# Optimization experiments

Measured on AMD Instinct MI355X. Metric: run time of the kernel, lower is better.

## Reference

```python
import jax, jax.numpy as jnp
import numpy as np

N_NODES = 50000
N_EDGES = 800000
IN_FEAT = 256
HEADS = 8
D_K = 64


def setup_inputs() -> dict:
    key = jax.random.key(0)
    ks = jax.random.split(key, 6)
    x = jax.random.normal(ks[0], (N_NODES, IN_FEAT), dtype=jnp.float32)
    edge_index = jax.random.randint(ks[1], (2, N_EDGES), 0, N_NODES, dtype=jnp.int32)
    # xavier-uniform linear weights, stored as [in, out] for x @ W
    limit = float(np.sqrt(6.0 / (IN_FEAT + HEADS * D_K)))
    Wq = jax.random.uniform(ks[2], (IN_FEAT, HEADS * D_K), jnp.float32, -limit, limit)
    Wk = jax.random.uniform(ks[3], (IN_FEAT, HEADS * D_K), jnp.float32, -limit, limit)
    Wv = jax.random.uniform(ks[4], (IN_FEAT, HEADS * D_K), jnp.float32, -limit, limit)
    D = jax.random.uniform(ks[5], (HEADS, D_K), jnp.float32, -1.0, 1.0)
    return {"x": x, "edge_index": edge_index, "Wq": Wq, "Wk": Wk, "Wv": Wv, "D": D}


def reference(x, edge_index, Wq, Wk, Wv, D):
    N = x.shape[0]
    H, dk = D.shape
    scale = 1.0 / np.sqrt(dk)

    Q = (x @ Wq).reshape(N, H, dk)
    K = (x @ Wk).reshape(N, H, dk)
    V = (x @ Wv).reshape(N, H, dk)

    row, col = edge_index[0], edge_index[1]
    Ke = K[row]          # [E, H, dk]
    Qe = Q[col]          # [E, H, dk] (for self edges col==row so Q[col]==Q[row])
    diff = Ke - Qe
    s_edge = jnp.einsum('ehd,hd->eh', diff * diff, D)   # diagonal Mahalanobis
    s_self = jnp.einsum('ehd,hd->eh', Ke * Qe, D)       # self-loop score
    scores = jnp.where((row == col)[:, None], s_self, s_edge)
    scores = jax.nn.leaky_relu(scores * scale, negative_slope=0.2)

    # segment softmax over destination node `row` (PyG softmax semantics)
    smax = jax.ops.segment_max(scores, row, num_segments=N)
    smax = jnp.where(jnp.isfinite(smax), smax, 0.0)     # nodes with no incoming edges
    ex = jnp.exp(scores - smax[row])
    denom = jax.ops.segment_sum(ex, row, num_segments=N)
    alpha = ex / (denom[row] + 1e-16)                   # [E, H]

    out = jax.ops.segment_sum(alpha[:, :, None] * V[col], row, num_segments=N)
    return out.reshape(N, H * dk)
```

## Files before the change

### kernel.cpp

```cpp
#include <hip/hip_runtime.h>
#include <hip/hip_bf16.h>

#define N_NODES 50000
#define N_PAD   50176
#define N_EDGES 800000
#define IN_FEAT 256
#define HEADS 8
#define D_K 64
#define HD 512

typedef __hip_bfloat16 bf16;
typedef unsigned int u32;

using bf16x8 = __attribute__((ext_vector_type(8))) short;
using f32x4  = __attribute__((ext_vector_type(4))) float;

#define WS_Q       0
#define WS_K       51200000
#define WS_V       102400000
#define WS_OFFSETS 153600000
#define WS_CURSOR  153800192
#define WS_DEG     154000192
#define WS_CSR     154200192
#define WS_SQ2     157400192
#define WS_AUX     159000192

#define DOUT_XB 0
#define DOUT_WT 25690112

#define SCAN_BLOCKS 49
#define EA_BLOCKS   1024

#define VMCNT0()   asm volatile("s_waitcnt vmcnt(0)" ::: "memory")
#define LGKMCNT0() asm volatile("s_waitcnt lgkmcnt(0)" ::: "memory")

__device__ __forceinline__ float bflo(u32 u) { return __uint_as_float(u << 16); }
__device__ __forceinline__ float bfhi(u32 u) { return __uint_as_float(u & 0xffff0000u); }

__device__ __forceinline__ void gload16(const void* g, void* l)
{
    __builtin_amdgcn_global_load_lds(
        (const __attribute__((address_space(1))) unsigned int*)g,
        (__attribute__((address_space(3))) unsigned int*)l,
        16, 0, 0);
}

__global__ __launch_bounds__(256) void convert_x(
    const float* __restrict__ x, bf16* __restrict__ xb)
{
    const int t   = blockIdx.x * 256 + threadIdx.x;
    const int row = t >> 5;
    const int c8  = (t & 31) * 8;
    if (row >= N_PAD) return;
    alignas(16) bf16 tmp[8];
    if (row < N_NODES) {
        const float* p = x + (size_t)row * IN_FEAT + c8;
        float4 a = *(const float4*)p;
        float4 b = *(const float4*)(p + 4);
        tmp[0] = __float2bfloat16(a.x); tmp[1] = __float2bfloat16(a.y);
        tmp[2] = __float2bfloat16(a.z); tmp[3] = __float2bfloat16(a.w);
        tmp[4] = __float2bfloat16(b.x); tmp[5] = __float2bfloat16(b.y);
        tmp[6] = __float2bfloat16(b.z); tmp[7] = __float2bfloat16(b.w);
    } else {
#pragma unroll
        for (int i = 0; i < 8; ++i) tmp[i] = __float2bfloat16(0.f);
    }
    *(uint4*)(xb + (size_t)row * IN_FEAT + c8) = *(const uint4*)tmp;
}

__global__ __launch_bounds__(256) void convert_w(
    const float* __restrict__ Wq, const float* __restrict__ Wk, const float* __restrict__ Wv,
    bf16* __restrict__ Wt)
{
    const int t = blockIdx.x * 256 + threadIdx.x;
    if (t >= 3 * 512 * 256) return;
    const int mat = t >> 17;
    const int r   = t & 131071;
    const int n   = r >> 8;
    const int k   = r & 255;
    const float* W = (mat == 0) ? Wq : (mat == 1) ? Wk : Wv;
    Wt[t] = __float2bfloat16(W[k * HD + n]);
}

__global__ __launch_bounds__(256) void mfma_qkv(
    const bf16* __restrict__ xb, const bf16* __restrict__ Wt,
    bf16* __restrict__ Qb, bf16* __restrict__ Kb, bf16* __restrict__ Vb)
{
    __shared__ uint4 Ab4[512];
    __shared__ uint4 Bb4[512];
    char* AbB = (char*)Ab4;
    char* BbB = (char*)Bb4;

    const int tid  = threadIdx.x;
    const int lane = tid & 63;
    const int wid  = tid >> 6;
    const int wr   = wid >> 1;
    const int wc   = wid & 1;

    const int m0  = blockIdx.x * 128;
    const int n0  = blockIdx.y * 128;
    const int mat = blockIdx.z;
    const bf16* __restrict__ wt = Wt + (size_t)mat * 512 * 256;
    bf16* __restrict__ outp = (mat == 0) ? Qb : (mat == 1) ? Kb : Vb;

    const int rch  = lane >> 2;
    const int slot = (lane & 3) ^ (rch & 3);
    const int sc0  = wid;
    const int sc1  = wid + 4;
    const size_t arow0 = (size_t)(m0 + sc0 * 16 + rch) * IN_FEAT + slot * 8;
    const size_t arow1 = (size_t)(m0 + sc1 * 16 + rch) * IN_FEAT + slot * 8;
    const size_t brow0 = (size_t)(n0 + sc0 * 16 + rch) * IN_FEAT + slot * 8;
    const size_t brow1 = (size_t)(n0 + sc1 * 16 + rch) * IN_FEAT + slot * 8;

    const int fr    = lane & 15;
    const int fslot = (((lane >> 4) ^ (lane & 3)) << 4);
    const int abase = (wr * 64 + fr) * 64 + fslot;
    const int bbase = (wc * 64 + fr) * 64 + fslot;

    f32x4 acc[4][4];
#pragma unroll
    for (int i = 0; i < 4; ++i)
#pragma unroll
        for (int j = 0; j < 4; ++j) acc[i][j] = {0.f, 0.f, 0.f, 0.f};

    for (int k0 = 0; k0 < IN_FEAT; k0 += 32) {
        gload16(xb + arow0 + k0, AbB + sc0 * 1024);
        gload16(xb + arow1 + k0, AbB + sc1 * 1024);
        gload16(wt + brow0 + k0, BbB + sc0 * 1024);
        gload16(wt + brow1 + k0, BbB + sc1 * 1024);
        __syncthreads();

        bf16x8 aF[4], bF[4];
#pragma unroll
        for (int m = 0; m < 4; ++m) aF[m] = *(const bf16x8*)(AbB + abase + m * 16 * 64);
#pragma unroll
        for (int n = 0; n < 4; ++n) bF[n] = *(const bf16x8*)(BbB + bbase + n * 16 * 64);
#pragma unroll
        for (int m = 0; m < 4; ++m)
#pragma unroll
            for (int n = 0; n < 4; ++n)
                acc[m][n] = __builtin_amdgcn_mfma_f32_16x16x32_bf16(aF[m], bF[n], acc[m][n], 0, 0, 0);
        __syncthreads();
    }

    const int c_col = lane & 15;
    const int r_hi  = (lane >> 4) * 4;
#pragma unroll
    for (int m = 0; m < 4; ++m) {
        const int grow_base = m0 + wr * 64 + m * 16 + r_hi;
#pragma unroll
        for (int j = 0; j < 4; ++j) {
            const int grow = grow_base + j;
            if (grow < N_NODES) {
#pragma unroll
                for (int n = 0; n < 4; ++n)
                    outp[(size_t)grow * HD + n0 + wc * 64 + n * 16 + c_col] =
                        __float2bfloat16(acc[m][n][j]);
            }
        }
    }
}

__global__ void zero_deg_kernel(int* __restrict__ deg)
{
    int i = blockIdx.x * 256 + threadIdx.x;
    if (i < N_NODES) deg[i] = 0;
}

__global__ void hist_kernel(const int* __restrict__ row, int* __restrict__ deg)
{
    int e = blockIdx.x * 256 + threadIdx.x;
    if (e < N_EDGES) atomicAdd(&deg[row[e]], 1);
}

__global__ __launch_bounds__(1024) void scan_local(const int* __restrict__ deg,
                                                   int* __restrict__ offsets,
                                                   int* __restrict__ aux)
{
    __shared__ int buf[1024];
    const int tid = threadIdx.x;
    const int i = blockIdx.x * 1024 + tid;
    const int v = (i < N_NODES) ? deg[i] : 0;
    buf[tid] = v;
    __syncthreads();
    for (int off = 1; off < 1024; off <<= 1) {
        int t = (tid >= off) ? buf[tid - off] : 0;
        __syncthreads();
        buf[tid] += t;
        __syncthreads();
    }
    if (i < N_NODES) offsets[i] = buf[tid] - v;
    if (tid == 1023) aux[blockIdx.x] = buf[1023];
}

__global__ void scan_aux(int* __restrict__ aux)
{
    const int tid = threadIdx.x;
    const int orig = (tid < SCAN_BLOCKS) ? aux[tid] : 0;
    int v = orig;
    for (int off = 1; off < 64; off <<= 1) {
        int t = __shfl_up(v, off, 64);
        if (tid >= off) v += t;
    }
    if (tid < SCAN_BLOCKS) aux[tid] = v - orig;
}

__global__ __launch_bounds__(1024) void scan_apply(const int* __restrict__ aux,
                                                   int* __restrict__ offsets,
                                                   int* __restrict__ cursor)
{
    const int i = blockIdx.x * 1024 + threadIdx.x;
    if (i < N_NODES) {
        const int off = offsets[i] + aux[i >> 10];
        offsets[i] = off;
        cursor[i]  = off;
    }
    if (i == 0) offsets[N_NODES] = N_EDGES;
}

__global__ void scatter_kernel(const int* __restrict__ row, const int* __restrict__ col,
                               int* __restrict__ cursor, int* __restrict__ csr_col)
{
    int e = blockIdx.x * 256 + threadIdx.x;
    if (e < N_EDGES) {
        const int pos = atomicAdd(&cursor[row[e]], 1);
        csr_col[pos] = col[e];
    }
}

__global__ __launch_bounds__(256) void sq2_kernel(
    const bf16* __restrict__ Qb, const float* __restrict__ Dm, float* __restrict__ sQ2)
{
    const int lane = threadIdx.x & 63;
    const int wid  = threadIdx.x >> 6;
    const int n = blockIdx.x * 4 + wid;
    if (n >= N_NODES) return;

    uint4 qp = *(const uint4*)(Qb + (size_t)n * HD + lane * 8);
    float4 da = *(const float4*)(Dm + lane * 8);
    float4 db = *(const float4*)(Dm + lane * 8 + 4);
    float q0 = bflo(qp.x), q1 = bfhi(qp.x), q2 = bflo(qp.y), q3 = bfhi(qp.y);
    float q4 = bflo(qp.z), q5 = bfhi(qp.z), q6 = bflo(qp.w), q7 = bfhi(qp.w);
    float s = da.x*q0*q0 + da.y*q1*q1 + da.z*q2*q2 + da.w*q3*q3
            + db.x*q4*q4 + db.y*q5*q5 + db.z*q6*q6 + db.w*q7*q7;
    s += __shfl_xor(s, 1, 64);
    s += __shfl_xor(s, 2, 64);
    s += __shfl_xor(s, 4, 64);
    if ((lane & 7) == 0) sQ2[n * 8 + (lane >> 3)] = s;
}

__global__ void edge_attn(
    const bf16* __restrict__ Qb, const bf16* __restrict__ Kb, const bf16* __restrict__ Vb,
    const float* __restrict__ Dm, const float* __restrict__ sQ2,
    const int* __restrict__ offsets, const int* __restrict__ csr_col,
    float* __restrict__ out)
{
    __shared__ uint4 qstage[4][8][64];
    __shared__ uint4 dk16[4][8][9];

    const int lane = threadIdx.x & 63;
    const int wid  = threadIdx.x >> 6;
    const int hA = lane & 7;
    const int jA = lane >> 3;
    const int hB = lane >> 3;

    const float4 da = *(const float4*)(Dm + lane * 8);
    const float4 db = *(const float4*)(Dm + lane * 8 + 4);

    uint4* qrow_lds = &qstage[wid][0][0];

    for (int r = blockIdx.x * 4 + wid; r < N_NODES; r += EA_BLOCKS * 4) {
        uint4 kp = *(const uint4*)(Kb + (size_t)r * HD + lane * 8);
        const float k0 = bflo(kp.x), k1 = bfhi(kp.x), k2 = bflo(kp.y), k3 = bfhi(kp.y);
        const float k4 = bflo(kp.z), k5 = bfhi(kp.z), k6 = bflo(kp.w), k7 = bfhi(kp.w);
        const float e0 = da.x*k0, e1 = da.y*k1, e2 = da.z*k2, e3 = da.w*k3;
        const float e4 = db.x*k4, e5 = db.y*k5, e6 = db.z*k6, e7 = db.w*k7;
        float sk = e0*k0 + e1*k1 + e2*k2 + e3*k3 + e4*k4 + e5*k5 + e6*k6 + e7*k7;
        sk += __shfl_xor(sk, 1, 64);
        sk += __shfl_xor(sk, 2, 64);
        sk += __shfl_xor(sk, 4, 64);
        {
            alignas(16) bf16 dkp[8];
            dkp[0] = __float2bfloat16(e0); dkp[1] = __float2bfloat16(e1);
            dkp[2] = __float2bfloat16(e2); dkp[3] = __float2bfloat16(e3);
            dkp[4] = __float2bfloat16(e4); dkp[5] = __float2bfloat16(e5);
            dkp[6] = __float2bfloat16(e6); dkp[7] = __float2bfloat16(e7);
            dk16[wid][lane >> 3][lane & 7] = *(const uint4*)dkp;
        }
        const float skA = __shfl(sk, hA * 8, 64);

        const int s0 = offsets[r];
        const int s1 = offsets[r + 1];
        const int nedge = s1 - s0;

        float m = -INFINITY, l = 0.f;
        float o0=0,o1=0,o2=0,o3=0,o4=0,o5=0,o6=0,o7=0;

        if (nedge > 0) {
            int cnt_cur = min(8, nedge);
            int cv_cur  = csr_col[s0 + min(lane, nedge - 1)];
#pragma unroll
            for (int e = 0; e < 8; ++e) {
                if (e < cnt_cur) {
                    const int ce = __shfl(cv_cur, e, 64);
                    gload16(Qb + (size_t)ce * HD + (size_t)((lane ^ e) * 8),
                            qrow_lds + e * 64);
                }
            }

            for (int eb = s0; eb < s1; eb += 8) {
                int cnt_nx = 0, cv_nx = 0;
                {
                    const int rem = s1 - (eb + 8);
                    if (rem > 0) { cnt_nx = min(8, rem); cv_nx = csr_col[eb + 8 + min(lane, rem - 1)]; }
                }

                VMCNT0();
                uint4 qp[8];
#pragma unroll
                for (int t = 0; t < 8; ++t)
                    qp[t] = qrow_lds[jA * 64 + ((hA * 8 + t) ^ jA)];
                LGKMCNT0();

#pragma unroll
                for (int e = 0; e < 8; ++e) {
                    if (e < cnt_nx) {
                        const int ce = __shfl(cv_nx, e, 64);
                        gload16(Qb + (size_t)ce * HD + (size_t)((lane ^ e) * 8),
                                qrow_lds + e * 64);
                    }
                }

                const int   my_ce = __shfl(cv_cur, jA, 64);
                const float sq2v  = sQ2[my_ce * 8 + hA];

                float cross = 0.f;
#pragma unroll
                for (int t = 0; t < 8; ++t) {
                    const uint4 qpv = qp[t];
                    const uint4 dq  = dk16[wid][hA][t];
                    cross += bflo(dq.x)*bflo(qpv.x) + bfhi(dq.x)*bfhi(qpv.x)
                           + bflo(dq.y)*bflo(qpv.y) + bfhi(dq.y)*bfhi(qpv.y)
                           + bflo(dq.z)*bflo(qpv.z) + bfhi(dq.z)*bfhi(qpv.z)
                           + bflo(dq.w)*bflo(qpv.w) + bfhi(dq.w)*bfhi(qpv.w);
                }

                const float sraw = (my_ce == r) ? cross : (skA - 2.f * cross + sq2v);
                const float y = sraw * 0.125f;
                float s = fmaxf(y, 0.2f * y);
                if (jA >= cnt_cur) s = -INFINITY;

                float bm = s;
                bm = fmaxf(bm, __shfl_xor(bm, 8, 64));
                bm = fmaxf(bm, __shfl_xor(bm, 16, 64));
                bm = fmaxf(bm, __shfl_xor(bm, 32, 64));
                const float mn   = fmaxf(m, bm);
                const float corr = __expf(m - mn);
                const float w    = __expf(s - mn);
                m = mn;
                float ls = w;
                ls += __shfl_xor(ls, 8, 64);
                ls += __shfl_xor(ls, 16, 64);
                ls += __shfl_xor(ls, 32, 64);
                l = l * corr + ls;
                const float corrB = __shfl(corr, hB, 64);
                o0*=corrB; o1*=corrB; o2*=corrB; o3*=corrB;
                o4*=corrB; o5*=corrB; o6*=corrB; o7*=corrB;

#pragma unroll
                for (int e = 0; e < 8; ++e) {
                    if (e < cnt_cur) {
                        const int   ce    = __shfl(cv_cur, e, 64);
                        const float alpha = __shfl(w, e * 8 + hB, 64);
                        const uint4 vp = *(const uint4*)(Vb + (size_t)ce * HD + lane * 8);
                        o0 = fmaf(alpha, bflo(vp.x), o0);
                        o1 = fmaf(alpha, bfhi(vp.x), o1);
                        o2 = fmaf(alpha, bflo(vp.y), o2);
                        o3 = fmaf(alpha, bfhi(vp.y), o3);
                        o4 = fmaf(alpha, bflo(vp.z), o4);
                        o5 = fmaf(alpha, bfhi(vp.z), o5);
                        o6 = fmaf(alpha, bflo(vp.w), o6);
                        o7 = fmaf(alpha, bfhi(vp.w), o7);
                    }
                }

                cv_cur = cv_nx; cnt_cur = cnt_nx;
            }
        }

        const float lB  = __shfl(l, hB, 64);
        const float inv = 1.f / (lB + 1e-16f);
        float4 r0 = {o0*inv, o1*inv, o2*inv, o3*inv};
        float4 r1 = {o4*inv, o5*inv, o6*inv, o7*inv};
        *(float4*)(out + (size_t)r * HD + lane * 8)     = r0;
        *(float4*)(out + (size_t)r * HD + lane * 8 + 4) = r1;
    }
}

extern "C" void kernel_launch(void* const* d_in, const int* in_sizes, int n_in,
                              void* d_out, int out_size, void* d_ws, size_t ws_size,
                              hipStream_t stream)
{
    const float* x  = (const float*)d_in[0];
    const int*   ei = (const int*)d_in[1];
    const float* Wq = (const float*)d_in[2];
    const float* Wk = (const float*)d_in[3];
    const float* Wv = (const float*)d_in[4];
    const float* Dm = (const float*)d_in[5];
    float* out = (float*)d_out;

    char* ws = (char*)d_ws;
    bf16* Qb      = (bf16*)(ws + WS_Q);
    bf16* Kb      = (bf16*)(ws + WS_K);
    bf16* Vb      = (bf16*)(ws + WS_V);
    int*  offsets = (int*)(ws + WS_OFFSETS);
    int*  cursor  = (int*)(ws + WS_CURSOR);
    int*  deg     = (int*)(ws + WS_DEG);
    int*  csr_col = (int*)(ws + WS_CSR);
    float* sQ2    = (float*)(ws + WS_SQ2);
    int*  aux     = (int*)(ws + WS_AUX);

    bf16* xb = (bf16*)((char*)d_out + DOUT_XB);
    bf16* Wt = (bf16*)((char*)d_out + DOUT_WT);

    const int* row = ei;
    const int* col = ei + N_EDGES;

    hipLaunchKernelGGL(zero_deg_kernel, dim3((N_NODES + 255) / 256), dim3(256), 0, stream, deg);
    hipLaunchKernelGGL(convert_x, dim3(N_PAD * 32 / 256), dim3(256), 0, stream, x, xb);
    hipLaunchKernelGGL(convert_w, dim3((3 * 512 * 256 + 255) / 256), dim3(256), 0, stream,
                       Wq, Wk, Wv, Wt);
    hipLaunchKernelGGL(hist_kernel, dim3((N_EDGES + 255) / 256), dim3(256), 0, stream, row, deg);
    hipLaunchKernelGGL(mfma_qkv, dim3(N_PAD / 128, 4, 3), dim3(256), 0, stream,
                       xb, Wt, Qb, Kb, Vb);
    hipLaunchKernelGGL(scan_local, dim3(SCAN_BLOCKS), dim3(1024), 0, stream, deg, offsets, aux);
    hipLaunchKernelGGL(scan_aux, dim3(1), dim3(64), 0, stream, aux);
    hipLaunchKernelGGL(scan_apply, dim3(SCAN_BLOCKS), dim3(1024), 0, stream, aux, offsets, cursor);
    hipLaunchKernelGGL(scatter_kernel, dim3((N_EDGES + 255) / 256), dim3(256), 0, stream,
                       row, col, cursor, csr_col);
    hipLaunchKernelGGL(sq2_kernel, dim3((N_NODES + 3) / 4), dim3(256), 0, stream, Qb, Dm, sQ2);
    hipLaunchKernelGGL(edge_attn, dim3(EA_BLOCKS), dim3(256), 0, stream,
                       Qb, Kb, Vb, Dm, sQ2, offsets, csr_col, out);
}
```

Baseline: 485.3 us.

## Double-buffer QKV GEMM tiles, register-prefetch Q rows in edge attention

The QKV MFMA GEMM now uses two LDS buffers, issuing the next k-tile's global-to-LDS loads before computing on the current one, with partial vmcnt waits and raw barriers. The edge attention kernel drops the LDS staging of neighbor Q rows and loads them straight into registers one batch ahead, with CSR column indices prefetched two batches ahead. The zero-degree kernel is replaced by hipMemsetAsync. These aim to hide global load latency, at the cost of more registers in both kernels and uncoalesced per-lane Q loads.

```diff
diff --git a/kernel.cpp b/kernel.cpp
--- a/kernel.cpp
+++ b/kernel.cpp
@@ -30,9 +30,6 @@
 
 #define SCAN_BLOCKS 49
 #define EA_BLOCKS   1024
-
-#define VMCNT0()   asm volatile("s_waitcnt vmcnt(0)" ::: "memory")
-#define LGKMCNT0() asm volatile("s_waitcnt lgkmcnt(0)" ::: "memory")
 
 __device__ __forceinline__ float bflo(u32 u) { return __uint_as_float(u << 16); }
 __device__ __forceinline__ float bfhi(u32 u) { return __uint_as_float(u & 0xffff0000u); }
@@ -86,10 +83,8 @@
     const bf16* __restrict__ xb, const bf16* __restrict__ Wt,
     bf16* __restrict__ Qb, bf16* __restrict__ Kb, bf16* __restrict__ Vb)
 {
-    __shared__ uint4 Ab4[512];
-    __shared__ uint4 Bb4[512];
-    char* AbB = (char*)Ab4;
-    char* BbB = (char*)Bb4;
+    __shared__ uint4 lds4[2048];
+    char* lds = (char*)lds4;
 
     const int tid  = threadIdx.x;
     const int lane = tid & 63;
@@ -123,25 +118,40 @@
 #pragma unroll
         for (int j = 0; j < 4; ++j) acc[i][j] = {0.f, 0.f, 0.f, 0.f};
 
-    for (int k0 = 0; k0 < IN_FEAT; k0 += 32) {
-        gload16(xb + arow0 + k0, AbB + sc0 * 1024);
-        gload16(xb + arow1 + k0, AbB + sc1 * 1024);
-        gload16(wt + brow0 + k0, BbB + sc0 * 1024);
-        gload16(wt + brow1 + k0, BbB + sc1 * 1024);
-        __syncthreads();
-
+#define STAGE(t, buf) do {                                              \
+        gload16(xb + arow0 + (t) * 32, lds + (buf) * 16384 + sc0 * 1024);          \
+        gload16(xb + arow1 + (t) * 32, lds + (buf) * 16384 + sc1 * 1024);          \
+        gload16(wt + brow0 + (t) * 32, lds + (buf) * 16384 + 8192 + sc0 * 1024);   \
+        gload16(wt + brow1 + (t) * 32, lds + (buf) * 16384 + 8192 + sc1 * 1024);   \
+    } while (0)
+
+    STAGE(0, 0);
+#pragma unroll
+    for (int t = 0; t < 8; ++t) {
+        const int cur = t & 1;
+        if (t < 7) {
+            STAGE(t + 1, cur ^ 1);
+            asm volatile("s_waitcnt vmcnt(4)" ::: "memory");
+        } else {
+            asm volatile("s_waitcnt vmcnt(0)" ::: "memory");
+        }
+        __builtin_amdgcn_s_barrier();
+
+        const char* A = lds + cur * 16384;
+        const char* B = A + 8192;
         bf16x8 aF[4], bF[4];
 #pragma unroll
-        for (int m = 0; m < 4; ++m) aF[m] = *(const bf16x8*)(AbB + abase + m * 16 * 64);
-#pragma unroll
-        for (int n = 0; n < 4; ++n) bF[n] = *(const bf16x8*)(BbB + bbase + n * 16 * 64);
+        for (int m = 0; m < 4; ++m) aF[m] = *(const bf16x8*)(A + abase + m * 1024);
+#pragma unroll
+        for (int n = 0; n < 4; ++n) bF[n] = *(const bf16x8*)(B + bbase + n * 1024);
 #pragma unroll
         for (int m = 0; m < 4; ++m)
 #pragma unroll
             for (int n = 0; n < 4; ++n)
                 acc[m][n] = __builtin_amdgcn_mfma_f32_16x16x32_bf16(aF[m], bF[n], acc[m][n], 0, 0, 0);
-        __syncthreads();
-    }
+        __builtin_amdgcn_s_barrier();
+    }
+#undef STAGE
 
     const int c_col = lane & 15;
     const int r_hi  = (lane >> 4) * 4;
@@ -159,12 +169,6 @@
             }
         }
     }
-}
-
-__global__ void zero_deg_kernel(int* __restrict__ deg)
-{
-    int i = blockIdx.x * 256 + threadIdx.x;
-    if (i < N_NODES) deg[i] = 0;
 }
 
 __global__ void hist_kernel(const int* __restrict__ row, int* __restrict__ deg)
@@ -255,7 +259,6 @@
     const int* __restrict__ offsets, const int* __restrict__ csr_col,
     float* __restrict__ out)
 {
-    __shared__ uint4 qstage[4][8][64];
     __shared__ uint4 dk16[4][8][9];
 
     const int lane = threadIdx.x & 63;
@@ -266,8 +269,6 @@
 
     const float4 da = *(const float4*)(Dm + lane * 8);
     const float4 db = *(const float4*)(Dm + lane * 8 + 4);
-
-    uint4* qrow_lds = &qstage[wid][0][0];
 
     for (int r = blockIdx.x * 4 + wid; r < N_NODES; r += EA_BLOCKS * 4) {
         uint4 kp = *(const uint4*)(Kb + (size_t)r * HD + lane * 8);
@@ -299,36 +300,33 @@
         if (nedge > 0) {
             int cnt_cur = min(8, nedge);
             int cv_cur  = csr_col[s0 + min(lane, nedge - 1)];
-#pragma unroll
-            for (int e = 0; e < 8; ++e) {
-                if (e < cnt_cur) {
-                    const int ce = __shfl(cv_cur, e, 64);
-                    gload16(Qb + (size_t)ce * HD + (size_t)((lane ^ e) * 8),
-                            qrow_lds + e * 64);
+            uint4 q[8];
+            {
+                const int myc = __shfl(cv_cur, jA, 64);
+                const bf16* qr = Qb + (size_t)myc * HD + hA * D_K;
+#pragma unroll
+                for (int t = 0; t < 8; ++t) q[t] = *(const uint4*)(qr + t * 8);
+            }
+            int cnt_nx = 0, cv_nx = 0;
+            {
+                const int rem = nedge - 8;
+                if (rem > 0) { cnt_nx = min(8, rem); cv_nx = csr_col[s0 + 8 + min(lane, rem - 1)]; }
+            }
+
+            for (int eb = s0; eb < s1; eb += 8) {
+                int cnt_n2 = 0, cv_n2 = 0;
+                {
+                    const int rem2 = s1 - (eb + 16);
+                    if (rem2 > 0) { cnt_n2 = min(8, rem2); cv_n2 = csr_col[eb + 16 + min(lane, rem2 - 1)]; }
                 }
-            }
-
-            for (int eb = s0; eb < s1; eb += 8) {
-                int cnt_nx = 0, cv_nx = 0;
-                {
-                    const int rem = s1 - (eb + 8);
-                    if (rem > 0) { cnt_nx = min(8, rem); cv_nx = csr_col[eb + 8 + min(lane, rem - 1)]; }
-                }
-
-                VMCNT0();
-                uint4 qp[8];
-#pragma unroll
-                for (int t = 0; t < 8; ++t)
-                    qp[t] = qrow_lds[jA * 64 + ((hA * 8 + t) ^ jA)];
-                LGKMCNT0();
-
-#pragma unroll
-                for (int e = 0; e < 8; ++e) {
-                    if (e < cnt_nx) {
-                        const int ce = __shfl(cv_nx, e, 64);
-                        gload16(Qb + (size_t)ce * HD + (size_t)((lane ^ e) * 8),
-                                qrow_lds + e * 64);
-                    }
+                uint4 qn[8];
+#pragma unroll
+                for (int t = 0; t < 8; ++t) qn[t] = q[t];
+                if (cnt_nx > 0) {
+                    const int mycn = __shfl(cv_nx, jA, 64);
+                    const bf16* qrn = Qb + (size_t)mycn * HD + hA * D_K;
+#pragma unroll
+                    for (int t = 0; t < 8; ++t) qn[t] = *(const uint4*)(qrn + t * 8);
                 }
 
                 const int   my_ce = __shfl(cv_cur, jA, 64);
@@ -337,12 +335,12 @@
                 float cross = 0.f;
 #pragma unroll
                 for (int t = 0; t < 8; ++t) {
-                    const uint4 qpv = qp[t];
-                    const uint4 dq  = dk16[wid][hA][t];
-                    cross += bflo(dq.x)*bflo(qpv.x) + bfhi(dq.x)*bfhi(qpv.x)
-                           + bflo(dq.y)*bflo(qpv.y) + bfhi(dq.y)*bfhi(qpv.y)
-                           + bflo(dq.z)*bflo(qpv.z) + bfhi(dq.z)*bfhi(qpv.z)
-                           + bflo(dq.w)*bflo(qpv.w) + bfhi(dq.w)*bfhi(qpv.w);
+                    const uint4 dq = dk16[wid][hA][t];
+                    const uint4 qv = q[t];
+                    cross += bflo(dq.x)*bflo(qv.x) + bfhi(dq.x)*bfhi(qv.x)
+                           + bflo(dq.y)*bflo(qv.y) + bfhi(dq.y)*bfhi(qv.y)
+                           + bflo(dq.z)*bflo(qv.z) + bfhi(dq.z)*bfhi(qv.z)
+                           + bflo(dq.w)*bflo(qv.w) + bfhi(dq.w)*bfhi(qv.w);
                 }
 
                 const float sraw = (my_ce == r) ? cross : (skA - 2.f * cross + sq2v);
@@ -384,7 +382,10 @@
                     }
                 }
 
+#pragma unroll
+                for (int t = 0; t < 8; ++t) q[t] = qn[t];
                 cv_cur = cv_nx; cnt_cur = cnt_nx;
+                cv_nx  = cv_n2; cnt_nx  = cnt_n2;
             }
         }
 
@@ -426,7 +427,7 @@
     const int* row = ei;
     const int* col = ei + N_EDGES;
 
-    hipLaunchKernelGGL(zero_deg_kernel, dim3((N_NODES + 255) / 256), dim3(256), 0, stream, deg);
+    hipMemsetAsync(deg, 0, N_NODES * sizeof(int), stream);
     hipLaunchKernelGGL(convert_x, dim3(N_PAD * 32 / 256), dim3(256), 0, stream, x, xb);
     hipLaunchKernelGGL(convert_w, dim3((3 * 512 * 256 + 255) / 256), dim3(256), 0, stream,
                        Wq, Wk, Wv, Wt);
```

After: 822.6 us. 1.69x slower.
